# Performance work log

Measured on AMD Instinct MI355X. Metric: run time of the kernel, lower is better.

## Reference

```python
import jax, jax.numpy as jnp
import numpy as np

NUM_ATOMS = 262144
INPUT_DIM = 256
HIDDEN_DIM = 256
NUM_HEADS = 8
HEAD_DIM = HIDDEN_DIM // NUM_HEADS
NUM_GRAPHS = 2048
SCALE = float(np.sqrt(HEAD_DIM))


def setup_inputs() -> dict:
    key = jax.random.key(0)
    ks = jax.random.split(key, 9)
    x = jax.random.normal(ks[0], (NUM_ATOMS, INPUT_DIM), dtype=jnp.float32)
    batch = jnp.sort(jax.random.randint(ks[1], (NUM_ATOMS,), 0, NUM_GRAPHS, dtype=jnp.int32))
    queries = jax.random.normal(ks[2], (NUM_HEADS, HEAD_DIM), dtype=jnp.float32)
    s_in = 1.0 / np.sqrt(INPUT_DIM)
    s_h = 1.0 / np.sqrt(HIDDEN_DIM)
    Wk = jax.random.uniform(ks[3], (INPUT_DIM, HIDDEN_DIM), jnp.float32, -s_in, s_in)
    bk = jax.random.uniform(ks[4], (HIDDEN_DIM,), jnp.float32, -s_in, s_in)
    Wv = jax.random.uniform(ks[5], (INPUT_DIM, HIDDEN_DIM), jnp.float32, -s_in, s_in)
    bv = jax.random.uniform(ks[6], (HIDDEN_DIM,), jnp.float32, -s_in, s_in)
    Wo = jax.random.uniform(ks[7], (HIDDEN_DIM, INPUT_DIM), jnp.float32, -s_h, s_h)
    bo = jax.random.uniform(ks[8], (INPUT_DIM,), jnp.float32, -s_h, s_h)
    return {"x": x, "batch": batch, "queries": queries, "Wk": Wk, "bk": bk,
            "Wv": Wv, "bv": bv, "Wo": Wo, "bo": bo}


def reference(x, batch, queries, Wk, bk, Wv, bv, Wo, bo):
    N = x.shape[0]
    # projections: [N, hidden] -> [N, H, D]
    keys = (x @ Wk + bk).reshape(N, NUM_HEADS, HEAD_DIM)
    values = (x @ Wv + bv).reshape(N, NUM_HEADS, HEAD_DIM)
    # per-node, per-head attention logits against learned queries
    scores = jnp.einsum('nhd,hd->nh', keys, queries) / SCALE  # [N, H]
    # segment-wise (per-graph) stable softmax over nodes
    seg_max = jax.ops.segment_max(scores, batch, num_segments=NUM_GRAPHS)  # [B, H]
    w = jnp.exp(scores - seg_max[batch])                                   # [N, H]
    denom = jax.ops.segment_sum(w, batch, num_segments=NUM_GRAPHS)         # [B, H]
    w = w / denom[batch]
    # weighted sum of values per graph: [B, H, D]
    attended = jax.ops.segment_sum(w[:, :, None] * values, batch, num_segments=NUM_GRAPHS)
    attended = attended.reshape(NUM_GRAPHS, HIDDEN_DIM)
    return attended @ Wo + bo  # [B, input_dim]
```

## Files before the change

kernel.cpp:

```cpp
#include <hip/hip_runtime.h>

#define N_ATOMS 262144
#define NGRAPH  2048
#define INV_SCALE 0.17677669529663687f

typedef float f32x2 __attribute__((ext_vector_type(2)));
typedef float f32x4 __attribute__((ext_vector_type(4)));

__device__ __forceinline__ f32x2 pk_mul(f32x2 a, f32x2 b) {
  f32x2 d; asm("v_pk_mul_f32 %0, %1, %2" : "=v"(d) : "v"(a), "v"(b)); return d;
}
__device__ __forceinline__ f32x2 pk_fma(f32x2 a, f32x2 b, f32x2 c) {
  f32x2 d; asm("v_pk_fma_f32 %0, %1, %2, %3" : "=v"(d) : "v"(a), "v"(b), "v"(c)); return d;
}
__device__ __forceinline__ f32x2 pk_fma_blo(f32x2 a, f32x2 b, f32x2 c) {
  f32x2 d; asm("v_pk_fma_f32 %0, %1, %2, %3 op_sel_hi:[0,1,1]"
               : "=v"(d) : "v"(a), "v"(b), "v"(c)); return d;
}
__device__ __forceinline__ f32x2 pk_fma_bhi(f32x2 a, f32x2 b, f32x2 c) {
  f32x2 d; asm("v_pk_fma_f32 %0, %1, %2, %3 op_sel:[1,0,0]"
               : "=v"(d) : "v"(a), "v"(b), "v"(c)); return d;
}
__device__ __forceinline__ f32x4 ldnt4(const float* p) {
  return __builtin_nontemporal_load(reinterpret_cast<const f32x4*>(p));
}

__global__ void k_pre(const float* __restrict__ Wk, const float* __restrict__ bk,
                      const float* __restrict__ q, const int* __restrict__ batch,
                      float* __restrict__ P, float* __restrict__ c,
                      int* __restrict__ bounds) {
  if (blockIdx.x < 8) {
    int h = blockIdx.x, i = threadIdx.x;
    float s = 0.f;
    #pragma unroll
    for (int d = 0; d < 32; ++d)
      s = fmaf(Wk[i * 256 + h * 32 + d], q[h * 32 + d], s);
    P[h * 256 + i] = s;
    if (i == 0) {
      float cc = 0.f;
      #pragma unroll
      for (int d = 0; d < 32; ++d) cc = fmaf(bk[h * 32 + d], q[h * 32 + d], cc);
      c[h] = cc;
    }
  } else {
    int g = (blockIdx.x - 8) * 256 + threadIdx.x;
    if (g >= NGRAPH) return;
    int lo = 0, hi = N_ATOMS;
    while (lo < hi) {
      int mid = (lo + hi) >> 1;
      if (batch[mid] < g) lo = mid + 1; else hi = mid;
    }
    bounds[2 * g] = lo;
    if (g > 0) bounds[2 * g - 1] = lo;
    if (g == NGRAPH - 1) bounds[2 * g + 1] = N_ATOMS;
  }
}

__device__ __forceinline__ float fold8(float acc[8], int lane) {
  {
    int m = lane & 8;
    float nw[4];
    #pragma unroll
    for (int j = 0; j < 4; ++j) {
      float snd = m ? acc[j] : acc[j + 4];
      float rcv = __shfl_xor(snd, 8, 64);
      nw[j] = (m ? acc[j + 4] : acc[j]) + rcv;
    }
    #pragma unroll
    for (int j = 0; j < 4; ++j) acc[j] = nw[j];
  }
  {
    int m = lane & 16;
    float nw[2];
    #pragma unroll
    for (int j = 0; j < 2; ++j) {
      float snd = m ? acc[j] : acc[j + 2];
      float rcv = __shfl_xor(snd, 16, 64);
      nw[j] = (m ? acc[j + 2] : acc[j]) + rcv;
    }
    acc[0] = nw[0]; acc[1] = nw[1];
  }
  float r;
  {
    int m = lane & 32;
    float snd = m ? acc[0] : acc[1];
    float rcv = __shfl_xor(snd, 32, 64);
    r = (m ? acc[1] : acc[0]) + rcv;
  }
  r += __shfl_xor(r, 1, 64);
  r += __shfl_xor(r, 2, 64);
  r += __shfl_xor(r, 4, 64);
  return r;
}

__global__ __launch_bounds__(256, 4) void k_fused(const float* __restrict__ x,
                                                  const float* __restrict__ P,
                                                  const float* __restrict__ c,
                                                  const int* __restrict__ bounds,
                                                  float* __restrict__ Ag) {
  int b = blockIdx.x;
  int s = bounds[2 * b], e = bounds[2 * b + 1];
  int t = threadIdx.x, lane = t & 63, wv = t >> 6;
  int h = ((lane >> 1) & 4) | ((lane >> 3) & 2) | ((lane >> 5) & 1);

  f32x2 Pl2[8][2];
  #pragma unroll
  for (int k = 0; k < 8; ++k) {
    f32x4 pv = *reinterpret_cast<const f32x4*>(P + k * 256 + 4 * lane);
    Pl2[k][0] = __builtin_shufflevector(pv, pv, 0, 1);
    Pl2[k][1] = __builtin_shufflevector(pv, pv, 2, 3);
  }
  float cl = c[h];

  f32x2 A2[8][2];
  #pragma unroll
  for (int k = 0; k < 8; ++k) { A2[k][0] = (f32x2)0.f; A2[k][1] = (f32x2)0.f; }
  float dacc = 0.f;

  __shared__ float elds[4][3][8];
  __shared__ float Asc[4][2][256];
  __shared__ float dws[4][8];
  __shared__ float dinvs[8];

  const float* xl = x + 4 * lane;

  auto ca = [&](int a) { return a < e ? a : (e - 1); };

  auto acc_step = [&](f32x4 XQ, int ES) {
    f32x4 eA = *reinterpret_cast<const f32x4*>(&elds[wv][ES][0]);
    f32x4 eB = *reinterpret_cast<const f32x4*>(&elds[wv][ES][4]);
    f32x2 ep[4] = { __builtin_shufflevector(eA, eA, 0, 1),
                    __builtin_shufflevector(eA, eA, 2, 3),
                    __builtin_shufflevector(eB, eB, 0, 1),
                    __builtin_shufflevector(eB, eB, 2, 3) };
    f32x2 xlo = __builtin_shufflevector(XQ, XQ, 0, 1);
    f32x2 xhi = __builtin_shufflevector(XQ, XQ, 2, 3);
    #pragma unroll
    for (int j = 0; j < 4; ++j) {
      A2[2*j][0]   = pk_fma_blo(ep[j], xlo, A2[2*j][0]);
      A2[2*j][1]   = pk_fma_blo(ep[j], xhi, A2[2*j][1]);
      A2[2*j+1][0] = pk_fma_bhi(ep[j], xlo, A2[2*j+1][0]);
      A2[2*j+1][1] = pk_fma_bhi(ep[j], xhi, A2[2*j+1][1]);
    }
  };

  auto dot_step = [&](f32x4 XQ, int ES, int aidx) {
    f32x2 xlo = __builtin_shufflevector(XQ, XQ, 0, 1);
    f32x2 xhi = __builtin_shufflevector(XQ, XQ, 2, 3);
    float acc[8];
    #pragma unroll
    for (int k = 0; k < 8; ++k) {
      f32x2 p = pk_fma(xhi, Pl2[k][1], pk_mul(xlo, Pl2[k][0]));
      acc[k] = p[0] + p[1];
    }
    float r = fold8(acc, lane);
    float ev = __expf((r + cl) * INV_SCALE);
    ev = (aidx < e) ? ev : 0.f;
    dacc += ev;
    if ((lane & 7) == 0) elds[wv][ES][h] = ev;
  };

  int i0 = s + wv;
  if (i0 < e) {
    int G = (e - i0 + 3) >> 2;
    int M = (G + 3) / 3;
    f32x4 xqA = ldnt4(xl + (size_t)ca(i0) * 256);
    f32x4 xqB = ldnt4(xl + (size_t)ca(i0 + 4) * 256);
    f32x4 xqC = {0.f, 0.f, 0.f, 0.f};
    if ((lane & 7) == 0) elds[wv][2][h] = 0.f;
    int a = i0;
    for (int m = 0; m < M; ++m) {
      acc_step(xqC, 2);
      xqC = ldnt4(xl + (size_t)ca(a + 8) * 256);
      dot_step(xqA, 0, a);
      acc_step(xqA, 0);
      xqA = ldnt4(xl + (size_t)ca(a + 12) * 256);
      dot_step(xqB, 1, a + 4);
      acc_step(xqB, 1);
      xqB = ldnt4(xl + (size_t)ca(a + 16) * 256);
      dot_step(xqC, 2, a + 8);
      a += 12;
    }
  }

  if ((lane & 7) == 0) dws[wv][h] = dacc;
  __syncthreads();
  if (t < 8) {
    float ds = dws[0][t] + dws[1][t] + dws[2][t] + dws[3][t];
    dinvs[t] = ds > 0.f ? 1.0f / ds : 0.f;
  }
  #pragma unroll
  for (int p = 0; p < 4; ++p) {
    float4 a0, a1;
    a0.x = A2[2*p][0][0];   a0.y = A2[2*p][0][1];
    a0.z = A2[2*p][1][0];   a0.w = A2[2*p][1][1];
    a1.x = A2[2*p+1][0][0]; a1.y = A2[2*p+1][0][1];
    a1.z = A2[2*p+1][1][0]; a1.w = A2[2*p+1][1][1];
    *reinterpret_cast<float4*>(&Asc[wv][0][4 * lane]) = a0;
    *reinterpret_cast<float4*>(&Asc[wv][1][4 * lane]) = a1;
    __syncthreads();
    float v0 = Asc[0][0][t] + Asc[1][0][t] + Asc[2][0][t] + Asc[3][0][t];
    float v1 = Asc[0][1][t] + Asc[1][1][t] + Asc[2][1][t] + Asc[3][1][t];
    Ag[(size_t)b * 2048 + (2*p) * 256 + t]   = v0 * dinvs[2*p];
    Ag[(size_t)b * 2048 + (2*p+1) * 256 + t] = v1 * dinvs[2*p+1];
    __syncthreads();
  }
}

__global__ __launch_bounds__(256) void k_out(const float* __restrict__ Ag,
                                             const int* __restrict__ bounds,
                                             const float* __restrict__ Wv,
                                             const float* __restrict__ bv,
                                             const float* __restrict__ Wo,
                                             const float* __restrict__ bo,
                                             float* __restrict__ out) {
  __shared__ float Alds[4 * 2048];
  __shared__ float attlds[4 * 256];
  __shared__ float eflag[4];
  int b0 = blockIdx.x * 4;
  int t = threadIdx.x;
  #pragma unroll
  for (int r = 0; r < 32; ++r) {
    int idx = r * 256 + t;
    Alds[idx] = Ag[(size_t)b0 * 2048 + idx];
  }
  if (t < 4) {
    int s = bounds[2 * (b0 + t)], e = bounds[2 * (b0 + t) + 1];
    eflag[t] = (e > s) ? 1.0f : 0.0f;
  }
  __syncthreads();
  int h = t >> 5;
  float bvk = bv[t];
  float acc[4];
  #pragma unroll
  for (int g = 0; g < 4; ++g) acc[g] = 0.f;
  for (int i4 = 0; i4 < 64; ++i4) {
    float aa[4][4];
    #pragma unroll
    for (int g = 0; g < 4; ++g) {
      float4 v = *reinterpret_cast<const float4*>(&Alds[g * 2048 + h * 256 + i4 * 4]);
      aa[g][0] = v.x; aa[g][1] = v.y; aa[g][2] = v.z; aa[g][3] = v.w;
    }
    #pragma unroll
    for (int j = 0; j < 4; ++j) {
      float wvv = Wv[(size_t)(i4 * 4 + j) * 256 + t];
      #pragma unroll
      for (int g = 0; g < 4; ++g) acc[g] = fmaf(aa[g][j], wvv, acc[g]);
    }
  }
  #pragma unroll
  for (int g = 0; g < 4; ++g) attlds[g * 256 + t] = acc[g] + bvk * eflag[g];
  __syncthreads();
  float boj = bo[t];
  float o[4];
  #pragma unroll
  for (int g = 0; g < 4; ++g) o[g] = boj;
  for (int k4 = 0; k4 < 64; ++k4) {
    float aa[4][4];
    #pragma unroll
    for (int g = 0; g < 4; ++g) {
      float4 v = *reinterpret_cast<const float4*>(&attlds[g * 256 + k4 * 4]);
      aa[g][0] = v.x; aa[g][1] = v.y; aa[g][2] = v.z; aa[g][3] = v.w;
    }
    #pragma unroll
    for (int j = 0; j < 4; ++j) {
      float wo = Wo[(size_t)(k4 * 4 + j) * 256 + t];
      #pragma unroll
      for (int g = 0; g < 4; ++g) o[g] = fmaf(aa[g][j], wo, o[g]);
    }
  }
  #pragma unroll
  for (int g = 0; g < 4; ++g) out[(size_t)(b0 + g) * 256 + t] = o[g];
}

extern "C" void kernel_launch(void* const* d_in, const int* in_sizes, int n_in,
                              void* d_out, int out_size, void* d_ws, size_t ws_size,
                              hipStream_t stream) {
  const float* x   = (const float*)d_in[0];
  const int*   bat = (const int*)d_in[1];
  const float* q   = (const float*)d_in[2];
  const float* Wk  = (const float*)d_in[3];
  const float* bk  = (const float*)d_in[4];
  const float* Wv  = (const float*)d_in[5];
  const float* bv  = (const float*)d_in[6];
  const float* Wo  = (const float*)d_in[7];
  const float* bo  = (const float*)d_in[8];
  float* out = (float*)d_out;

  float* ws = (float*)d_ws;
  float* P      = ws;
  float* c      = ws + 2048;
  int*   bounds = (int*)(ws + 4096);
  float* Ag     = ws + 8192;

  k_pre<<<16, 256, 0, stream>>>(Wk, bk, q, bat, P, c, bounds);
  k_fused<<<NGRAPH, 256, 0, stream>>>(x, P, c, bounds, Ag);
  k_out<<<NGRAPH / 4, 256, 0, stream>>>(Ag, bounds, Wv, bv, Wo, bo, out);
}
```

Measured before the change: 101.8 us.

## Split heads across wave pairs in 512-thread blocks and drop manual prefetch

The fused kernel now launches 512 threads per graph. Each pair of waves covers the same atoms, and each wave owns four of the eight heads, which halves per-thread accumulator and projection registers and lets more waves be resident. The three-stage software-pipelined loop with nontemporal loads and clamped indices is replaced by a plain strided loop with ordinary loads. The shuffle reduction and the cross-wave LDS reduction are adjusted to match. In exchange, every x row is now read by two waves, and latency hiding depends on occupancy rather than explicit prefetch.

```diff
diff --git a/kernel.cpp b/kernel.cpp
--- a/kernel.cpp
+++ b/kernel.cpp
@@ -20,9 +20,6 @@
 __device__ __forceinline__ f32x2 pk_fma_bhi(f32x2 a, f32x2 b, f32x2 c) {
   f32x2 d; asm("v_pk_fma_f32 %0, %1, %2, %3 op_sel:[1,0,0]"
                : "=v"(d) : "v"(a), "v"(b), "v"(c)); return d;
-}
-__device__ __forceinline__ f32x4 ldnt4(const float* p) {
-  return __builtin_nontemporal_load(reinterpret_cast<const f32x4*>(p));
 }
 
 __global__ void k_pre(const float* __restrict__ Wk, const float* __restrict__ bk,
@@ -56,19 +53,7 @@
   }
 }
 
-__device__ __forceinline__ float fold8(float acc[8], int lane) {
-  {
-    int m = lane & 8;
-    float nw[4];
-    #pragma unroll
-    for (int j = 0; j < 4; ++j) {
-      float snd = m ? acc[j] : acc[j + 4];
-      float rcv = __shfl_xor(snd, 8, 64);
-      nw[j] = (m ? acc[j + 4] : acc[j]) + rcv;
-    }
-    #pragma unroll
-    for (int j = 0; j < 4; ++j) acc[j] = nw[j];
-  }
+__device__ __forceinline__ float fold4(float acc[4], int lane) {
   {
     int m = lane & 16;
     float nw[2];
@@ -90,10 +75,11 @@
   r += __shfl_xor(r, 1, 64);
   r += __shfl_xor(r, 2, 64);
   r += __shfl_xor(r, 4, 64);
+  r += __shfl_xor(r, 8, 64);
   return r;
 }
 
-__global__ __launch_bounds__(256, 4) void k_fused(const float* __restrict__ x,
+__global__ __launch_bounds__(512, 8) void k_fused(const float* __restrict__ x,
                                                   const float* __restrict__ P,
                                                   const float* __restrict__ c,
                                                   const int* __restrict__ bounds,
@@ -101,108 +87,78 @@
   int b = blockIdx.x;
   int s = bounds[2 * b], e = bounds[2 * b + 1];
   int t = threadIdx.x, lane = t & 63, wv = t >> 6;
-  int h = ((lane >> 1) & 4) | ((lane >> 3) & 2) | ((lane >> 5) & 1);
-
-  f32x2 Pl2[8][2];
-  #pragma unroll
-  for (int k = 0; k < 8; ++k) {
-    f32x4 pv = *reinterpret_cast<const f32x4*>(P + k * 256 + 4 * lane);
+  int hh = wv & 1, ar = wv >> 1;
+  int hl = ((lane >> 3) & 2) | ((lane >> 5) & 1);
+
+  f32x2 Pl2[4][2];
+  #pragma unroll
+  for (int k = 0; k < 4; ++k) {
+    f32x4 pv = *reinterpret_cast<const f32x4*>(P + (hh * 4 + k) * 256 + 4 * lane);
     Pl2[k][0] = __builtin_shufflevector(pv, pv, 0, 1);
     Pl2[k][1] = __builtin_shufflevector(pv, pv, 2, 3);
   }
-  float cl = c[h];
-
-  f32x2 A2[8][2];
-  #pragma unroll
-  for (int k = 0; k < 8; ++k) { A2[k][0] = (f32x2)0.f; A2[k][1] = (f32x2)0.f; }
+  float cl = c[hh * 4 + hl];
+
+  f32x2 A2[4][2];
+  #pragma unroll
+  for (int k = 0; k < 4; ++k) { A2[k][0] = (f32x2)0.f; A2[k][1] = (f32x2)0.f; }
   float dacc = 0.f;
 
-  __shared__ float elds[4][3][8];
-  __shared__ float Asc[4][2][256];
-  __shared__ float dws[4][8];
+  __shared__ float elds[8][4];
+  __shared__ float Asc[8][256];
+  __shared__ float dws[8][4];
   __shared__ float dinvs[8];
 
-  const float* xl = x + 4 * lane;
-
-  auto ca = [&](int a) { return a < e ? a : (e - 1); };
-
-  auto acc_step = [&](f32x4 XQ, int ES) {
-    f32x4 eA = *reinterpret_cast<const f32x4*>(&elds[wv][ES][0]);
-    f32x4 eB = *reinterpret_cast<const f32x4*>(&elds[wv][ES][4]);
-    f32x2 ep[4] = { __builtin_shufflevector(eA, eA, 0, 1),
-                    __builtin_shufflevector(eA, eA, 2, 3),
-                    __builtin_shufflevector(eB, eB, 0, 1),
-                    __builtin_shufflevector(eB, eB, 2, 3) };
-    f32x2 xlo = __builtin_shufflevector(XQ, XQ, 0, 1);
-    f32x2 xhi = __builtin_shufflevector(XQ, XQ, 2, 3);
-    #pragma unroll
-    for (int j = 0; j < 4; ++j) {
-      A2[2*j][0]   = pk_fma_blo(ep[j], xlo, A2[2*j][0]);
-      A2[2*j][1]   = pk_fma_blo(ep[j], xhi, A2[2*j][1]);
-      A2[2*j+1][0] = pk_fma_bhi(ep[j], xlo, A2[2*j+1][0]);
-      A2[2*j+1][1] = pk_fma_bhi(ep[j], xhi, A2[2*j+1][1]);
-    }
-  };
-
-  auto dot_step = [&](f32x4 XQ, int ES, int aidx) {
-    f32x2 xlo = __builtin_shufflevector(XQ, XQ, 0, 1);
-    f32x2 xhi = __builtin_shufflevector(XQ, XQ, 2, 3);
-    float acc[8];
-    #pragma unroll
-    for (int k = 0; k < 8; ++k) {
+  for (int n = s + ar; n < e; n += 4) {
+    f32x4 xq = *reinterpret_cast<const f32x4*>(x + (size_t)n * 256 + 4 * lane);
+    f32x2 xlo = __builtin_shufflevector(xq, xq, 0, 1);
+    f32x2 xhi = __builtin_shufflevector(xq, xq, 2, 3);
+
+    float acc[4];
+    #pragma unroll
+    for (int k = 0; k < 4; ++k) {
       f32x2 p = pk_fma(xhi, Pl2[k][1], pk_mul(xlo, Pl2[k][0]));
       acc[k] = p[0] + p[1];
     }
-    float r = fold8(acc, lane);
+    float r = fold4(acc, lane);
     float ev = __expf((r + cl) * INV_SCALE);
-    ev = (aidx < e) ? ev : 0.f;
     dacc += ev;
-    if ((lane & 7) == 0) elds[wv][ES][h] = ev;
-  };
-
-  int i0 = s + wv;
-  if (i0 < e) {
-    int G = (e - i0 + 3) >> 2;
-    int M = (G + 3) / 3;
-    f32x4 xqA = ldnt4(xl + (size_t)ca(i0) * 256);
-    f32x4 xqB = ldnt4(xl + (size_t)ca(i0 + 4) * 256);
-    f32x4 xqC = {0.f, 0.f, 0.f, 0.f};
-    if ((lane & 7) == 0) elds[wv][2][h] = 0.f;
-    int a = i0;
-    for (int m = 0; m < M; ++m) {
-      acc_step(xqC, 2);
-      xqC = ldnt4(xl + (size_t)ca(a + 8) * 256);
-      dot_step(xqA, 0, a);
-      acc_step(xqA, 0);
-      xqA = ldnt4(xl + (size_t)ca(a + 12) * 256);
-      dot_step(xqB, 1, a + 4);
-      acc_step(xqB, 1);
-      xqB = ldnt4(xl + (size_t)ca(a + 16) * 256);
-      dot_step(xqC, 2, a + 8);
-      a += 12;
-    }
-  }
-
-  if ((lane & 7) == 0) dws[wv][h] = dacc;
+
+    if ((lane & 15) == 0) elds[wv][hl] = ev;
+    f32x4 e4 = *reinterpret_cast<const f32x4*>(&elds[wv][0]);
+    f32x2 ep0 = __builtin_shufflevector(e4, e4, 0, 1);
+    f32x2 ep1 = __builtin_shufflevector(e4, e4, 2, 3);
+    A2[0][0] = pk_fma_blo(ep0, xlo, A2[0][0]);
+    A2[0][1] = pk_fma_blo(ep0, xhi, A2[0][1]);
+    A2[1][0] = pk_fma_bhi(ep0, xlo, A2[1][0]);
+    A2[1][1] = pk_fma_bhi(ep0, xhi, A2[1][1]);
+    A2[2][0] = pk_fma_blo(ep1, xlo, A2[2][0]);
+    A2[2][1] = pk_fma_blo(ep1, xhi, A2[2][1]);
+    A2[3][0] = pk_fma_bhi(ep1, xlo, A2[3][0]);
+    A2[3][1] = pk_fma_bhi(ep1, xhi, A2[3][1]);
+  }
+
+  if ((lane & 15) == 0) dws[wv][hl] = dacc;
   __syncthreads();
   if (t < 8) {
-    float ds = dws[0][t] + dws[1][t] + dws[2][t] + dws[3][t];
+    int hhg = t >> 2, hlg = t & 3;
+    float ds = dws[hhg][hlg] + dws[hhg + 2][hlg] +
+               dws[hhg + 4][hlg] + dws[hhg + 6][hlg];
     dinvs[t] = ds > 0.f ? 1.0f / ds : 0.f;
   }
+  __syncthreads();
+  int col = t & 255, which = t >> 8;
   #pragma unroll
   for (int p = 0; p < 4; ++p) {
-    float4 a0, a1;
-    a0.x = A2[2*p][0][0];   a0.y = A2[2*p][0][1];
-    a0.z = A2[2*p][1][0];   a0.w = A2[2*p][1][1];
-    a1.x = A2[2*p+1][0][0]; a1.y = A2[2*p+1][0][1];
-    a1.z = A2[2*p+1][1][0]; a1.w = A2[2*p+1][1][1];
-    *reinterpret_cast<float4*>(&Asc[wv][0][4 * lane]) = a0;
-    *reinterpret_cast<float4*>(&Asc[wv][1][4 * lane]) = a1;
+    float4 av;
+    av.x = A2[p][0][0]; av.y = A2[p][0][1];
+    av.z = A2[p][1][0]; av.w = A2[p][1][1];
+    *reinterpret_cast<float4*>(&Asc[wv][4 * lane]) = av;
     __syncthreads();
-    float v0 = Asc[0][0][t] + Asc[1][0][t] + Asc[2][0][t] + Asc[3][0][t];
-    float v1 = Asc[0][1][t] + Asc[1][1][t] + Asc[2][1][t] + Asc[3][1][t];
-    Ag[(size_t)b * 2048 + (2*p) * 256 + t]   = v0 * dinvs[2*p];
-    Ag[(size_t)b * 2048 + (2*p+1) * 256 + t] = v1 * dinvs[2*p+1];
+    float v = Asc[which][col] + Asc[which + 2][col] +
+              Asc[which + 4][col] + Asc[which + 6][col];
+    int g = which * 4 + p;
+    Ag[(size_t)b * 2048 + (size_t)g * 256 + col] = v * dinvs[g];
     __syncthreads();
   }
 }
@@ -294,6 +250,6 @@
   float* Ag     = ws + 8192;
 
   k_pre<<<16, 256, 0, stream>>>(Wk, bk, q, bat, P, c, bounds);
-  k_fused<<<NGRAPH, 256, 0, stream>>>(x, P, c, bounds, Ag);
+  k_fused<<<NGRAPH, 512, 0, stream>>>(x, P, c, bounds, Ag);
   k_out<<<NGRAPH / 4, 256, 0, stream>>>(Ag, bounds, Wv, bv, Wo, bo, out);
 }
```

After: 118.8 us. +16.7%, slower.
